# Optimization experiments

Hardware: AMD Instinct MI355X
Metric: run time of the kernel (lower is better)

The kernel has to match this reference:

```python
import jax, jax.numpy as jnp
import numpy as np

HEAD, DIM_IN, HDIM = 8, 256, 64
B, N = 4, 2048


def setup_inputs() -> dict:
    key = jax.random.key(0)
    k1, k2, k3, k4 = jax.random.split(key, 4)
    # xavier_uniform gain=1.414 bounds
    def xavier(k, shape, fan_in, fan_out):
        bound = 1.414 * np.sqrt(6.0 / (fan_in + fan_out))
        return jax.random.uniform(k, shape, jnp.float32, -bound, bound)
    h = jax.random.normal(k1, (B, N, DIM_IN), jnp.float32)
    w = xavier(k2, (HEAD, DIM_IN, HDIM), DIM_IN, HDIM)
    a_src = xavier(k3, (HEAD, HDIM, 1), HDIM, 1)
    a_dst = xavier(k4, (HEAD, HDIM, 1), HDIM, 1)
    b = jnp.zeros((HDIM,), jnp.float32)
    return {"h": h, "w": w, "a_src": a_src, "a_dst": a_dst, "b": b}


def reference(h, w, a_src, a_dst, b):
    # h: [B,N,Din], w: [H,Din,O] -> h_: [B,H,N,O]
    h_ = jnp.einsum("bnd,hdo->bhno", h, w)
    # additive attention logits per node: [B,H,N]
    src = jnp.einsum("bhno,ho->bhn", h_, a_src[..., 0])
    dst = jnp.einsum("bhno,ho->bhn", h_, a_dst[..., 0])
    # attn[b,h,i,j] = leaky_relu(src[i] + dst[j]); softmax over j
    logits = jax.nn.leaky_relu(src[..., :, None] + dst[..., None, :], negative_slope=0.2)
    attn = jax.nn.softmax(logits, axis=-1)  # [B,H,N,N]
    h_out = jnp.einsum("bhij,bhjo->bhio", attn, h_)
    return h_out + b
```

## Files before the change

### kernel.cpp

```cpp
#include <hip/hip_runtime.h>
#include <cstdint>
#include <cstddef>


#define HEADS 8
#define DIN   256
#define HDIM  64
#define NN    2048

typedef __attribute__((ext_vector_type(8))) _Float16 f16x8;
typedef __attribute__((ext_vector_type(2))) _Float16 f16x2;
typedef __attribute__((ext_vector_type(2))) __fp16   fp16x2;
typedef __attribute__((ext_vector_type(4))) float f32x4;

union H8 { f16x8 v; f16x2 p[4]; unsigned u[4]; };
union F2U { f16x2 h; fp16x2 q; unsigned u; };

__device__ __forceinline__ f16x2 pkrtz(float a, float b) {
  F2U t; t.q = __builtin_amdgcn_cvt_pkrtz(a, b);
  return t.h;
}
__device__ __forceinline__ unsigned pkrtz_u(float a, float b) {
  F2U t; t.q = __builtin_amdgcn_cvt_pkrtz(a, b);
  return t.u;
}

__global__ __launch_bounds__(256) void gat_prep(const float* __restrict__ w,
                                                const float* __restrict__ h,
                                                _Float16* __restrict__ wt,
                                                _Float16* __restrict__ hc) {
  const int bid = blockIdx.x;
  if (bid < 512) {
    const int idx = bid * 256 + threadIdx.x;
    const int o  = idx & 63;
    const int k  = (idx >> 6) & 255;
    const int hd = idx >> 14;
    wt[(hd * HDIM + o) * DIN + k] = (_Float16)w[idx];
  } else {
    const int idx = (bid - 512) * 256 + threadIdx.x;
    const float* p = h + (size_t)idx * 8;
    float4 x0 = ((const float4*)p)[0];
    float4 x1 = ((const float4*)p)[1];
    H8 o;
    o.p[0] = pkrtz(x0.x, x0.y); o.p[1] = pkrtz(x0.z, x0.w);
    o.p[2] = pkrtz(x1.x, x1.y); o.p[3] = pkrtz(x1.z, x1.w);
    *(f16x8*)(hc + (size_t)idx * 8) = o.v;
  }
}

__global__ __launch_bounds__(256) void gat_proj(const _Float16* __restrict__ hc,
                                                const _Float16* __restrict__ wt,
                                                const float* __restrict__ a_src,
                                                const float* __restrict__ a_dst,
                                                _Float16* __restrict__ h_t,
                                                float* __restrict__ src_s,
                                                float* __restrict__ dst_s) {
  const int head = blockIdx.x;
  const int rt   = blockIdx.y;
  const int tid  = threadIdx.x;
  const int w    = tid >> 6;
  const int lane = tid & 63;
  const int l15  = lane & 15, lg = lane >> 4;

  const int rowg = rt * 128 + w * 32;
  const _Float16* hb = hc + (size_t)rowg * DIN;
  const _Float16* wb = wt + head * (HDIM * DIN);

  f32x4 acc[2][4] = {};

  f16x8 Aa0, Aa1, Ab0, Ab1, Ab2, Ab3;
  f16x8 Ba0, Ba1, Bb0, Bb1, Bb2, Bb3;

#define LDP(S, kk) do {                                                \
    const int k0_ = (kk) * 32 + lg * 8;                                \
    S##a0 = *(const f16x8*)(hb + (size_t)(l15) * DIN + k0_);           \
    S##a1 = *(const f16x8*)(hb + (size_t)(16 + l15) * DIN + k0_);      \
    S##b0 = *(const f16x8*)(wb + (size_t)(l15) * DIN + k0_);           \
    S##b1 = *(const f16x8*)(wb + (size_t)(16 + l15) * DIN + k0_);      \
    S##b2 = *(const f16x8*)(wb + (size_t)(32 + l15) * DIN + k0_);      \
    S##b3 = *(const f16x8*)(wb + (size_t)(48 + l15) * DIN + k0_);      \
  } while (0)

#define MMP(S) do {                                                    \
    acc[0][0] = __builtin_amdgcn_mfma_f32_16x16x32_f16(S##a0, S##b0, acc[0][0], 0, 0, 0); \
    acc[0][1] = __builtin_amdgcn_mfma_f32_16x16x32_f16(S##a0, S##b1, acc[0][1], 0, 0, 0); \
    acc[0][2] = __builtin_amdgcn_mfma_f32_16x16x32_f16(S##a0, S##b2, acc[0][2], 0, 0, 0); \
    acc[0][3] = __builtin_amdgcn_mfma_f32_16x16x32_f16(S##a0, S##b3, acc[0][3], 0, 0, 0); \
    acc[1][0] = __builtin_amdgcn_mfma_f32_16x16x32_f16(S##a1, S##b0, acc[1][0], 0, 0, 0); \
    acc[1][1] = __builtin_amdgcn_mfma_f32_16x16x32_f16(S##a1, S##b1, acc[1][1], 0, 0, 0); \
    acc[1][2] = __builtin_amdgcn_mfma_f32_16x16x32_f16(S##a1, S##b2, acc[1][2], 0, 0, 0); \
    acc[1][3] = __builtin_amdgcn_mfma_f32_16x16x32_f16(S##a1, S##b3, acc[1][3], 0, 0, 0); \
  } while (0)

  LDP(A, 0);
#pragma unroll
  for (int kk = 0; kk < 6; kk += 2) {
    LDP(B, kk + 1);
    MMP(A);
    LDP(A, kk + 2);
    MMP(B);
  }
  LDP(B, 7);
  MMP(A);
  MMP(B);

#undef LDP
#undef MMP

  const int b   = (rt * 128) >> 11;
  const int nl0 = ((rt * 128) & 2047) + w * 32;
  const int bh  = b * HEADS + head;
  _Float16* hb_t = h_t + (size_t)bh * (256 * 512);
#pragma unroll
  for (int m = 0; m < 2; ++m)
#pragma unroll
    for (int n = 0; n < 4; ++n) {
      uint2 pk;
      pk.x = pkrtz_u(acc[m][n][0], acc[m][n][1]);
      pk.y = pkrtz_u(acc[m][n][2], acc[m][n][3]);
      const int j0 = nl0 + m * 16 + lg * 4;
      const int o  = n * 16 + l15;
      *(uint2*)(hb_t + (size_t)(j0 >> 3) * 512 + o * 8 + (j0 & 7)) = pk;
    }

  const float LOG2E = 1.4426950408889634f;
  float as4[4], ad4[4];
#pragma unroll
  for (int n = 0; n < 4; ++n) {
    as4[n] = a_src[head * HDIM + n * 16 + l15];
    ad4[n] = a_dst[head * HDIM + n * 16 + l15];
  }
#pragma unroll
  for (int m = 0; m < 2; ++m)
#pragma unroll
    for (int reg = 0; reg < 4; ++reg) {
      float ps = 0.f, pd = 0.f;
#pragma unroll
      for (int n = 0; n < 4; ++n) {
        float c = acc[m][n][reg];
        ps = fmaf(c, as4[n], ps);
        pd = fmaf(c, ad4[n], pd);
      }
#pragma unroll
      for (int off = 1; off <= 8; off <<= 1) {
        ps += __shfl_xor(ps, off);
        pd += __shfl_xor(pd, off);
      }
      if (l15 == 0) {
        const int nl = nl0 + m * 16 + lg * 4 + reg;
        src_s[(size_t)bh * NN + nl] = ps * LOG2E;
        dst_s[(size_t)bh * NN + nl] = pd * LOG2E;
      }
    }
}

__global__ __launch_bounds__(256) void gat_flash(const float* __restrict__ src_s,
                                                 const float* __restrict__ dst_s,
                                                 const _Float16* __restrict__ h_t,
                                                 const float* __restrict__ bias,
                                                 float* __restrict__ out) {
  const int it  = blockIdx.x;
  const int bh  = blockIdx.y;
  const int tid = threadIdx.x;
  const int w   = tid >> 6;
  const int lane = tid & 63;
  const int l15 = lane & 15, lg = lane >> 4;

  __shared__ _Float16 Ef[NN];
  __shared__ _Float16 Ff[NN];
  __shared__ float red[4];

  const float* dstp = dst_s + (size_t)bh * NN;
  const _Float16* vpan = h_t + (size_t)bh * (256 * 512);
  const _Float16* fb = vpan + lg * 512 + l15 * 8;

  float d[8];
  {
    float4 q0 = *(const float4*)(dstp + tid * 8);
    float4 q1 = *(const float4*)(dstp + tid * 8 + 4);
    d[0]=q0.x; d[1]=q0.y; d[2]=q0.z; d[3]=q0.w;
    d[4]=q1.x; d[5]=q1.y; d[6]=q1.z; d[7]=q1.w;
  }
  float dm = fmaxf(fmaxf(fmaxf(d[0],d[1]),fmaxf(d[2],d[3])),
                   fmaxf(fmaxf(d[4],d[5]),fmaxf(d[6],d[7])));
#pragma unroll
  for (int off = 32; off >= 1; off >>= 1) dm = fmaxf(dm, __shfl_xor(dm, off));
  if (lane == 0) red[w] = dm;
  __syncthreads();
  dm = fmaxf(fmaxf(red[0], red[1]), fmaxf(red[2], red[3]));

  {
    H8 e8, f8;
#pragma unroll
    for (int k = 0; k < 4; ++k) {
      float a0 = d[2*k]   - dm;
      float a1 = d[2*k+1] - dm;
      e8.p[k] = pkrtz(__builtin_amdgcn_exp2f(a0), __builtin_amdgcn_exp2f(a1));
      f8.p[k] = pkrtz(__builtin_amdgcn_exp2f(0.2f * a0),
                      __builtin_amdgcn_exp2f(0.2f * a1));
    }
    *(f16x8*)(&Ef[tid * 8]) = e8.v;
    *(f16x8*)(&Ff[tid * 8]) = f8.v;
  }
  __syncthreads();

  const float* srcp = src_s + (size_t)bh * NN + it * 128 + w * 32;
  f16x2 u2[2], v2[2];
#pragma unroll
  for (int m = 0; m < 2; ++m) {
    float sv   = srcp[m * 16 + l15];
    float smax = sv + dm;
    float mi   = fmaxf(smax, 0.2f * smax);
    float u    = __builtin_amdgcn_exp2f(smax - mi);
    float v    = __builtin_amdgcn_exp2f(fmaf(0.2f, smax, -mi));
    u2[m] = pkrtz(u, u);
    v2[m] = pkrtz(v, v);
  }

  f32x4 acc[2][4] = {};
  f32x4 accs[2]   = {};
  H8 onesU; onesU.u[0] = onesU.u[1] = onesU.u[2] = onesU.u[3] = 0x3C003C00u;
  const f16x8 ones = onesU.v;

  f16x8 V00, V01, V02, V03, V10, V11, V12, V13;
  f16x8 V20, V21, V22, V23, V30, V31, V32, V33;

#define LOADV(s, jc) do {                                              \
    const _Float16* fp_ = fb + (size_t)(jc) * 2048;                    \
    V##s##0 = *(const f16x8*)(fp_);                                    \
    V##s##1 = *(const f16x8*)(fp_ + 128);                              \
    V##s##2 = *(const f16x8*)(fp_ + 256);                              \
    V##s##3 = *(const f16x8*)(fp_ + 384);                              \
  } while (0)

#define STEP(s, jc) do {                                               \
    H8 eu_, fu_;                                                       \
    eu_.v = *(const f16x8*)(&Ef[(jc) * 32 + lg * 8]);                  \
    fu_.v = *(const f16x8*)(&Ff[(jc) * 32 + lg * 8]);                  \
    _Pragma("unroll") for (int m = 0; m < 2; ++m) {                    \
      H8 af_;                                                          \
      af_.p[0] = __builtin_elementwise_max(u2[m] * eu_.p[0], v2[m] * fu_.p[0]); \
      af_.p[1] = __builtin_elementwise_max(u2[m] * eu_.p[1], v2[m] * fu_.p[1]); \
      af_.p[2] = __builtin_elementwise_max(u2[m] * eu_.p[2], v2[m] * fu_.p[2]); \
      af_.p[3] = __builtin_elementwise_max(u2[m] * eu_.p[3], v2[m] * fu_.p[3]); \
      acc[m][0] = __builtin_amdgcn_mfma_f32_16x16x32_f16(af_.v, V##s##0, acc[m][0], 0, 0, 0); \
      acc[m][1] = __builtin_amdgcn_mfma_f32_16x16x32_f16(af_.v, V##s##1, acc[m][1], 0, 0, 0); \
      acc[m][2] = __builtin_amdgcn_mfma_f32_16x16x32_f16(af_.v, V##s##2, acc[m][2], 0, 0, 0); \
      acc[m][3] = __builtin_amdgcn_mfma_f32_16x16x32_f16(af_.v, V##s##3, acc[m][3], 0, 0, 0); \
      accs[m]   = __builtin_amdgcn_mfma_f32_16x16x32_f16(af_.v, ones, accs[m], 0, 0, 0);      \
    }                                                                  \
  } while (0)

  LOADV(0, 0);
  LOADV(1, 1);
  LOADV(2, 2);
#pragma unroll 1
  for (int t = 0; t < 60; t += 4) {
    LOADV(3, t + 3); STEP(0, t);
    LOADV(0, t + 4); STEP(1, t + 1);
    LOADV(1, t + 5); STEP(2, t + 2);
    LOADV(2, t + 6); STEP(3, t + 3);
  }
  LOADV(3, 63);
  STEP(0, 60); STEP(1, 61); STEP(2, 62); STEP(3, 63);

#undef LOADV
#undef STEP

  float bb[4];
#pragma unroll
  for (int n = 0; n < 4; ++n) bb[n] = bias[n * 16 + l15];

  float* ob = out + ((size_t)bh * NN + it * 128 + w * 32) * HDIM;
#pragma unroll
  for (int m = 0; m < 2; ++m)
#pragma unroll
    for (int reg = 0; reg < 4; ++reg) {
      const float linv = 1.0f / accs[m][reg];
      const int r = m * 16 + lg * 4 + reg;
#pragma unroll
      for (int n = 0; n < 4; ++n)
        ob[(size_t)r * HDIM + n * 16 + l15] = fmaf(acc[m][n][reg], linv, bb[n]);
    }
}

extern "C" void kernel_launch(void* const* d_in, const int* in_sizes, int n_in,
                              void* d_out, int out_size, void* d_ws, size_t ws_size,
                              hipStream_t stream) {
  const float* h     = (const float*)d_in[0];
  const float* w     = (const float*)d_in[1];
  const float* a_src = (const float*)d_in[2];
  const float* a_dst = (const float*)d_in[3];
  const float* bias  = (const float*)d_in[4];
  float* out = (float*)d_out;

  char* ws = (char*)d_ws;
  _Float16* wt  = (_Float16*)ws;
  _Float16* h_t = (_Float16*)(ws + 262144);
  float* src_s = (float*)(ws + 262144 + 8388608);
  float* dst_s = (float*)(ws + 262144 + 8388608 + 262144);

  _Float16* hcv = (_Float16*)d_out;

  hipLaunchKernelGGL(gat_prep,  dim3(1536),   dim3(256), 0, stream, w, h, wt, hcv);
  hipLaunchKernelGGL(gat_proj,  dim3(8, 64),  dim3(256), 0, stream,
                     hcv, wt, a_src, a_dst, h_t, src_s, dst_s);
  hipLaunchKernelGGL(gat_flash, dim3(16, 32), dim3(256), 0, stream,
                     src_s, dst_s, h_t, bias, out);
}
```

Measured before the change: 49.53 us.

## Split key range across wave pairs in flash kernel and reduce via LDS

Each block now covers 64 query rows instead of 128. Each pair of waves splits the 2048-key range in half, and the partial output and row-sum accumulators are combined through shared memory before the epilogue. The grid doubles to 1024 blocks, the V prefetch depth drops from three stages to two to save registers, and launch bounds request 4 blocks per CU. The aim is more occupancy and parallelism on the attention kernel. In exchange, each block recomputes the dst exponent table, adds extra LDS traffic and a barrier, and leaves half the waves idle during the epilogue.

```diff
diff --git a/kernel.cpp b/kernel.cpp
--- a/kernel.cpp
+++ b/kernel.cpp
@@ -154,25 +154,30 @@
     }
 }
 
-__global__ __launch_bounds__(256) void gat_flash(const float* __restrict__ src_s,
-                                                 const float* __restrict__ dst_s,
-                                                 const _Float16* __restrict__ h_t,
-                                                 const float* __restrict__ bias,
-                                                 float* __restrict__ out) {
+__global__ __launch_bounds__(256, 4) void gat_flash(const float* __restrict__ src_s,
+                                                    const float* __restrict__ dst_s,
+                                                    const _Float16* __restrict__ h_t,
+                                                    const float* __restrict__ bias,
+                                                    float* __restrict__ out) {
   const int it  = blockIdx.x;
   const int bh  = blockIdx.y;
   const int tid = threadIdx.x;
   const int w   = tid >> 6;
   const int lane = tid & 63;
   const int l15 = lane & 15, lg = lane >> 4;
+  const int rg  = w >> 1;
+  const int jh  = w & 1;
 
   __shared__ _Float16 Ef[NN];
   __shared__ _Float16 Ff[NN];
+  __shared__ f32x4 Oc[2][2][4][64];
+  __shared__ f32x4 Sc[2][2][64];
   __shared__ float red[4];
 
   const float* dstp = dst_s + (size_t)bh * NN;
   const _Float16* vpan = h_t + (size_t)bh * (256 * 512);
   const _Float16* fb = vpan + lg * 512 + l15 * 8;
+  const int jb = jh * 32;
 
   float d[8];
   {
@@ -204,7 +209,7 @@
   }
   __syncthreads();
 
-  const float* srcp = src_s + (size_t)bh * NN + it * 128 + w * 32;
+  const float* srcp = src_s + (size_t)bh * NN + it * 64 + rg * 32;
   f16x2 u2[2], v2[2];
 #pragma unroll
   for (int m = 0; m < 2; ++m) {
@@ -223,7 +228,6 @@
   const f16x8 ones = onesU.v;
 
   f16x8 V00, V01, V02, V03, V10, V11, V12, V13;
-  f16x8 V20, V21, V22, V23, V30, V31, V32, V33;
 
 #define LOADV(s, jc) do {                                              \
     const _Float16* fp_ = fb + (size_t)(jc) * 2048;                    \
@@ -251,37 +255,51 @@
     }                                                                  \
   } while (0)
 
-  LOADV(0, 0);
-  LOADV(1, 1);
-  LOADV(2, 2);
+  LOADV(0, jb + 0);
+  LOADV(1, jb + 1);
 #pragma unroll 1
-  for (int t = 0; t < 60; t += 4) {
-    LOADV(3, t + 3); STEP(0, t);
-    LOADV(0, t + 4); STEP(1, t + 1);
-    LOADV(1, t + 5); STEP(2, t + 2);
-    LOADV(2, t + 6); STEP(3, t + 3);
-  }
-  LOADV(3, 63);
-  STEP(0, 60); STEP(1, 61); STEP(2, 62); STEP(3, 63);
+  for (int t = 0; t < 28; t += 2) {
+    STEP(0, jb + t);     LOADV(0, jb + t + 2);
+    STEP(1, jb + t + 1); LOADV(1, jb + t + 3);
+  }
+  STEP(0, jb + 28); LOADV(0, jb + 30);
+  STEP(1, jb + 29); LOADV(1, jb + 31);
+  STEP(0, jb + 30);
+  STEP(1, jb + 31);
 
 #undef LOADV
 #undef STEP
 
-  float bb[4];
-#pragma unroll
-  for (int n = 0; n < 4; ++n) bb[n] = bias[n * 16 + l15];
-
-  float* ob = out + ((size_t)bh * NN + it * 128 + w * 32) * HDIM;
-#pragma unroll
-  for (int m = 0; m < 2; ++m)
-#pragma unroll
-    for (int reg = 0; reg < 4; ++reg) {
-      const float linv = 1.0f / accs[m][reg];
-      const int r = m * 16 + lg * 4 + reg;
-#pragma unroll
-      for (int n = 0; n < 4; ++n)
-        ob[(size_t)r * HDIM + n * 16 + l15] = fmaf(acc[m][n][reg], linv, bb[n]);
-    }
+  if (jh == 1) {
+#pragma unroll
+    for (int m = 0; m < 2; ++m) {
+      Sc[rg][m][lane] = accs[m];
+#pragma unroll
+      for (int n = 0; n < 4; ++n) Oc[rg][m][n][lane] = acc[m][n];
+    }
+  }
+  __syncthreads();
+  if (jh == 0) {
+    float bb[4];
+#pragma unroll
+    for (int n = 0; n < 4; ++n) bb[n] = bias[n * 16 + l15];
+
+    float* ob = out + ((size_t)bh * NN + it * 64 + rg * 32) * HDIM;
+#pragma unroll
+    for (int m = 0; m < 2; ++m) {
+      f32x4 st = accs[m] + Sc[rg][m][lane];
+#pragma unroll
+      for (int reg = 0; reg < 4; ++reg) {
+        const float linv = 1.0f / st[reg];
+        const int r = m * 16 + lg * 4 + reg;
+#pragma unroll
+        for (int n = 0; n < 4; ++n) {
+          float o = acc[m][n][reg] + Oc[rg][m][n][lane][reg];
+          ob[(size_t)r * HDIM + n * 16 + l15] = fmaf(o, linv, bb[n]);
+        }
+      }
+    }
+  }
 }
 
 extern "C" void kernel_launch(void* const* d_in, const int* in_sizes, int n_in,
@@ -305,6 +323,6 @@
   hipLaunchKernelGGL(gat_prep,  dim3(1536),   dim3(256), 0, stream, w, h, wt, hcv);
   hipLaunchKernelGGL(gat_proj,  dim3(8, 64),  dim3(256), 0, stream,
                      hcv, wt, a_src, a_dst, h_t, src_s, dst_s);
-  hipLaunchKernelGGL(gat_flash, dim3(16, 32), dim3(256), 0, stream,
+  hipLaunchKernelGGL(gat_flash, dim3(32, 32), dim3(256), 0, stream,
                      src_s, dst_s, h_t, bias, out);
 }
```

Result: slower. 50.88 us (+2.7%).
